# Kernel tuning notes

Measured on AMD Instinct MI355X. Metric: run time of the kernel, lower is better.

Reference implementation:

```python
import jax, jax.numpy as jnp
import numpy as np

INPUT_SIZE = 1024
HIDDEN_SIZE = 2048
BATCH = 4096


def _xavier(key, shape):
    fan_out, fan_in = shape
    std = jnp.sqrt(2.0 / (fan_in + fan_out)).astype(jnp.float32)
    return jax.random.normal(key, shape, dtype=jnp.float32) * std


def setup_inputs() -> dict:
    key = jax.random.key(0)
    ks = jax.random.split(key, 8)
    return {
        "x": jax.random.normal(ks[0], (BATCH, INPUT_SIZE), dtype=jnp.float32),
        "hprev": jax.random.normal(ks[1], (BATCH, HIDDEN_SIZE), dtype=jnp.float32),
        "Wh": _xavier(ks[2], (HIDDEN_SIZE, INPUT_SIZE)),
        "Wz": _xavier(ks[3], (HIDDEN_SIZE, INPUT_SIZE)),
        "Wr": _xavier(ks[4], (HIDDEN_SIZE, INPUT_SIZE)),
        "Uh": _xavier(ks[5], (HIDDEN_SIZE, HIDDEN_SIZE)),
        "Uz": _xavier(ks[6], (HIDDEN_SIZE, HIDDEN_SIZE)),
        "Ur": _xavier(ks[7], (HIDDEN_SIZE, HIDDEN_SIZE)),
        "bh": jnp.zeros((HIDDEN_SIZE,), dtype=jnp.float32),
        "bz": jnp.zeros((HIDDEN_SIZE,), dtype=jnp.float32),
        "br": jnp.zeros((HIDDEN_SIZE,), dtype=jnp.float32),
    }


def reference(x, hprev, Wh, Wz, Wr, Uh, Uz, Ur, bh, bz, br):
    # batched matvec: (b,i) @ (h,i)^T -> (b,h)
    r = jax.nn.sigmoid(x @ Wr.T + hprev @ Ur.T + br)
    z = jax.nn.sigmoid(x @ Wz.T + hprev @ Uz.T + bz)
    h_proposed = jnp.tanh(x @ Wh.T + (r * hprev) @ Uh.T + bh)
    return z * h_proposed + (1.0 - z) * hprev
```

## Files before the change

kernel.cpp:

```cpp
#include <hip/hip_runtime.h>

#define BATCH 4096
#define ISZ   1024
#define HSZ   2048

typedef __bf16 bf16x8 __attribute__((ext_vector_type(8)));
typedef float  f32x4  __attribute__((ext_vector_type(4)));

__device__ __forceinline__ unsigned short f2bf(float f) {
  unsigned u = __builtin_bit_cast(unsigned, f);
  u += 0x7fffu + ((u >> 16) & 1u);
  return (unsigned short)(u >> 16);
}
__device__ __forceinline__ float bf2f(unsigned short s) {
  unsigned u = ((unsigned)s) << 16;
  return __builtin_bit_cast(float, u);
}

struct CvtArgs {
  const float* src[6];
  unsigned short* dst[6];
  int cum[7];
};

__global__ __launch_bounds__(256) void cvt_all_kernel(CvtArgs a, int total4) {
  int i = blockIdx.x * 256 + threadIdx.x;
  if (i >= total4) return;
  int s = 0;
#pragma unroll
  for (int k = 0; k < 5; ++k) s += (i >= a.cum[k + 1]) ? 1 : 0;
  int off = i - a.cum[s];
  float4 f = ((const float4*)a.src[s])[off];
  ushort4 o;
  o.x = f2bf(f.x); o.y = f2bf(f.y); o.z = f2bf(f.z); o.w = f2bf(f.w);
  ((ushort4*)a.dst[s])[off] = o;
}

__device__ __forceinline__ void stage_tile64(const unsigned short* __restrict__ g, int ldK,
                                             int tileRow, int k0, char* lds, int t) {
  char* l0 = lds + ((t >> 6) << 10);
#pragma unroll
  for (int k = 0; k < 4; ++k) {
    int linear = t + k * 256;
    int row = linear >> 3;
    int cs  = linear & 7;
    int c   = cs ^ (row & 7);
    const unsigned short* gp = g + (size_t)(tileRow + row) * ldK + (k0 + c * 8);
    __builtin_amdgcn_global_load_lds((const __attribute__((address_space(1))) void*)gp,
                                     (__attribute__((address_space(3))) void*)(l0 + k * 4096),
                                     16, 0, 0);
  }
}

__device__ __forceinline__ void stage_tile64_w8(const unsigned short* __restrict__ g, int ldK,
                                                int tileRow, int k0, char* lds, int t) {
  char* l0 = lds + ((t >> 6) << 10);
#pragma unroll
  for (int k = 0; k < 2; ++k) {
    int linear = t + k * 512;
    int row = linear >> 3;
    int cs  = linear & 7;
    int c   = cs ^ (row & 7);
    const unsigned short* gp = g + (size_t)(tileRow + row) * ldK + (k0 + c * 8);
    __builtin_amdgcn_global_load_lds((const __attribute__((address_space(1))) void*)gp,
                                     (__attribute__((address_space(3))) void*)(l0 + k * 8192),
                                     16, 0, 0);
  }
}

__device__ __forceinline__ void gemm_seg(const unsigned short* __restrict__ A,
                                         const unsigned short* __restrict__ W,
                                         int K, int rowBase, int colBase,
                                         char* ldsA, char* ldsB,
                                         f32x4 (&acc)[4][4], int t) {
  const int lane = t & 63;
  const int wid  = t >> 6;
  const int wm   = wid >> 1, wn = wid & 1;
  const int lrow = lane & 15;
  const int quad = lane >> 4;
  const int r7   = lrow & 7;
  for (int k0 = 0; k0 < K; k0 += 64) {
    stage_tile64(A, K, rowBase, k0, ldsA, t);
    stage_tile64(W, K, colBase, k0, ldsB, t);
    __syncthreads();
#pragma unroll
    for (int kk = 0; kk < 2; ++kk) {
      const int swz = (((kk << 2) | quad) ^ r7) * 16;
      bf16x8 af[4], bfr[4];
#pragma unroll
      for (int i = 0; i < 4; ++i) {
        af[i]  = *(const bf16x8*)(ldsA + (wm * 64 + i * 16 + lrow) * 128 + swz);
        bfr[i] = *(const bf16x8*)(ldsB + (wn * 64 + i * 16 + lrow) * 128 + swz);
      }
#pragma unroll
      for (int i = 0; i < 4; ++i)
#pragma unroll
        for (int j = 0; j < 4; ++j)
          acc[i][j] = __builtin_amdgcn_mfma_f32_16x16x32_bf16(af[i], bfr[j], acc[i][j], 0, 0, 0);
    }
    __syncthreads();
  }
}

__device__ __forceinline__ void gemm_seg8(const unsigned short* __restrict__ A,
                                          const unsigned short* __restrict__ W,
                                          int K, int rowBase, int colBase,
                                          char* ldsA, char* ldsB,
                                          f32x4 (&acc)[4][2], int t) {
  const int lane = t & 63;
  const int wid  = t >> 6;
  const int wm   = wid >> 2;
  const int wn   = wid & 3;
  const int lrow = lane & 15;
  const int quad = lane >> 4;
  const int r7   = lrow & 7;
  for (int k0 = 0; k0 < K; k0 += 64) {
    stage_tile64_w8(A, K, rowBase, k0, ldsA, t);
    stage_tile64_w8(W, K, colBase, k0, ldsB, t);
    __syncthreads();
#pragma unroll
    for (int kk = 0; kk < 2; ++kk) {
      const int swz = (((kk << 2) | quad) ^ r7) * 16;
      bf16x8 af[4], bfr[2];
#pragma unroll
      for (int i = 0; i < 4; ++i)
        af[i]  = *(const bf16x8*)(ldsA + (wm * 64 + i * 16 + lrow) * 128 + swz);
#pragma unroll
      for (int j = 0; j < 2; ++j)
        bfr[j] = *(const bf16x8*)(ldsB + (wn * 32 + j * 16 + lrow) * 128 + swz);
#pragma unroll
      for (int i = 0; i < 4; ++i)
#pragma unroll
        for (int j = 0; j < 2; ++j)
          acc[i][j] = __builtin_amdgcn_mfma_f32_16x16x32_bf16(af[i], bfr[j], acc[i][j], 0, 0, 0);
    }
    __syncthreads();
  }
}

__device__ __forceinline__ float fast_sigmoid(float v) {
  return 1.0f / (1.0f + __expf(-v));
}
__device__ __forceinline__ float fast_tanh(float v) {
  float e = __expf(2.0f * v);
  return 1.0f - 2.0f / (e + 1.0f);
}

__global__ __launch_bounds__(256, 4) void gate_rz(
    const unsigned short* __restrict__ xb, const unsigned short* __restrict__ hb,
    const unsigned short* __restrict__ Wr, const unsigned short* __restrict__ Ur,
    const unsigned short* __restrict__ Wz, const unsigned short* __restrict__ Uz,
    const float* __restrict__ br, const float* __restrict__ bz,
    const float* __restrict__ Wh32, const float* __restrict__ Uh32,
    unsigned short* __restrict__ Whb, unsigned short* __restrict__ Uhb,
    unsigned short* __restrict__ rh, unsigned short* __restrict__ Zbuf) {
  __shared__ char lds[32768];
  const int t = threadIdx.x;

  if (blockIdx.z == 0) {
    const int NW = (HSZ * ISZ) / 4;
    const int NU = (HSZ * HSZ) / 4;
    int tid = (blockIdx.x + (blockIdx.y << 4)) * 256 + t;
    for (int i = tid; i < NW + NU; i += 512 * 256) {
      const float4* s4 = (i < NW) ? (const float4*)Wh32 + i
                                  : (const float4*)Uh32 + (i - NW);
      ushort4* d4 = (i < NW) ? (ushort4*)Whb + i
                             : (ushort4*)Uhb + (i - NW);
      float4 f = *s4;
      ushort4 o;
      o.x = f2bf(f.x); o.y = f2bf(f.y); o.z = f2bf(f.z); o.w = f2bf(f.w);
      *d4 = o;
    }
    return;
  }

  char* ldsA = lds;
  char* ldsB = lds + 16384;
  int lin = blockIdx.x + (blockIdx.y << 4) + ((blockIdx.z - 1) << 9);
  int xcd = lin & 7, s = lin >> 3;
  int bx = xcd * 2 + (s & 1);
  int by = (s >> 1) & 31;
  int bz_ = s >> 6;

  const int rowBase = by * 128;
  const int colBase = bx * 128;
  const bool isZ = (bz_ != 0);
  const unsigned short* W = isZ ? Wz : Wr;
  const unsigned short* U = isZ ? Uz : Ur;
  const float* biasP = isZ ? bz : br;

  f32x4 acc[4][4];
#pragma unroll
  for (int i = 0; i < 4; ++i)
#pragma unroll
    for (int j = 0; j < 4; ++j)
      acc[i][j] = (f32x4){0.f, 0.f, 0.f, 0.f};

  gemm_seg(xb, W, ISZ, rowBase, colBase, ldsA, ldsB, acc, t);
  gemm_seg(hb, U, HSZ, rowBase, colBase, ldsA, ldsB, acc, t);

  const int lane = t & 63, wid = t >> 6;
  const int wm = wid >> 1, wn = wid & 1, lrow = lane & 15, quad = lane >> 4;
#pragma unroll
  for (int i = 0; i < 4; ++i) {
#pragma unroll
    for (int j = 0; j < 4; ++j) {
      int col = colBase + wn * 64 + j * 16 + lrow;
      float bv = biasP[col];
#pragma unroll
      for (int r = 0; r < 4; ++r) {
        int row = rowBase + wm * 64 + i * 16 + quad * 4 + r;
        float sg = fast_sigmoid(acc[i][j][r] + bv);
        int idx = row * HSZ + col;
        if (isZ) {
          Zbuf[idx] = f2bf(sg);
        } else {
          rh[idx] = f2bf(sg * bf2f(hb[idx]));
        }
      }
    }
  }
}

__global__ __launch_bounds__(512, 4) void gate_h(
    const unsigned short* __restrict__ xb, const unsigned short* __restrict__ rhb,
    const unsigned short* __restrict__ Wh, const unsigned short* __restrict__ Uh,
    const float* __restrict__ bh, const unsigned short* __restrict__ Zbuf,
    const float* __restrict__ hprev, float* __restrict__ out) {
  __shared__ char lds[32768];
  char* ldsA = lds;
  char* ldsB = lds + 16384;
  const int t = threadIdx.x;

  int lin = blockIdx.x + (blockIdx.y << 4);
  int xcd = lin & 7, s = lin >> 3;
  int bx = xcd * 2 + (s & 1);
  int by = s >> 1;

  const int rowBase = by * 128;
  const int colBase = bx * 128;

  f32x4 acc[4][2];
#pragma unroll
  for (int i = 0; i < 4; ++i)
#pragma unroll
    for (int j = 0; j < 2; ++j)
      acc[i][j] = (f32x4){0.f, 0.f, 0.f, 0.f};

  gemm_seg8(xb, Wh, ISZ, rowBase, colBase, ldsA, ldsB, acc, t);
  gemm_seg8(rhb, Uh, HSZ, rowBase, colBase, ldsA, ldsB, acc, t);

  const int lane = t & 63, wid = t >> 6;
  const int wm = wid >> 2, wn = wid & 3, lrow = lane & 15, quad = lane >> 4;
#pragma unroll
  for (int i = 0; i < 4; ++i) {
#pragma unroll
    for (int j = 0; j < 2; ++j) {
      int col = colBase + wn * 32 + j * 16 + lrow;
      float bv = bh[col];
#pragma unroll
      for (int r = 0; r < 4; ++r) {
        int row = rowBase + wm * 64 + i * 16 + quad * 4 + r;
        float hp = fast_tanh(acc[i][j][r] + bv);
        int idx = row * HSZ + col;
        float z = bf2f(Zbuf[idx]);
        float h = hprev[idx];
        out[idx] = h + z * (hp - h);
      }
    }
  }
}

extern "C" void kernel_launch(void* const* d_in, const int* in_sizes, int n_in,
                              void* d_out, int out_size, void* d_ws, size_t ws_size,
                              hipStream_t stream) {
  (void)in_sizes; (void)n_in; (void)out_size; (void)ws_size;
  const float* x     = (const float*)d_in[0];
  const float* hprev = (const float*)d_in[1];
  const float* Wh    = (const float*)d_in[2];
  const float* Wz    = (const float*)d_in[3];
  const float* Wr    = (const float*)d_in[4];
  const float* Uh    = (const float*)d_in[5];
  const float* Uz    = (const float*)d_in[6];
  const float* Ur    = (const float*)d_in[7];
  const float* bh    = (const float*)d_in[8];
  const float* bz    = (const float*)d_in[9];
  const float* br    = (const float*)d_in[10];
  float* out = (float*)d_out;

  char* ws = (char*)d_ws;
  size_t off = 0;
  auto alloc = [&](size_t bytes) { char* p = ws + off; off += bytes; return p; };
  unsigned short* xb  = (unsigned short*)alloc((size_t)BATCH * ISZ * 2);
  unsigned short* hb  = (unsigned short*)alloc((size_t)BATCH * HSZ * 2);
  unsigned short* Wrb = (unsigned short*)alloc((size_t)HSZ * ISZ * 2);
  unsigned short* Wzb = (unsigned short*)alloc((size_t)HSZ * ISZ * 2);
  unsigned short* Whb = (unsigned short*)alloc((size_t)HSZ * ISZ * 2);
  unsigned short* Urb = (unsigned short*)alloc((size_t)HSZ * HSZ * 2);
  unsigned short* Uzb = (unsigned short*)alloc((size_t)HSZ * HSZ * 2);
  unsigned short* Uhb = (unsigned short*)alloc((size_t)HSZ * HSZ * 2);
  unsigned short* rhb = (unsigned short*)alloc((size_t)BATCH * HSZ * 2);
  unsigned short* Zb  = (unsigned short*)alloc((size_t)BATCH * HSZ * 2);

  CvtArgs ca;
  const float* srcs[6]      = {x, hprev, Wr, Wz, Ur, Uz};
  unsigned short* dsts[6]   = {xb, hb, Wrb, Wzb, Urb, Uzb};
  int n4s[6] = {BATCH * ISZ / 4, BATCH * HSZ / 4,
                HSZ * ISZ / 4, HSZ * ISZ / 4,
                HSZ * HSZ / 4, HSZ * HSZ / 4};
  int cum = 0;
  for (int i = 0; i < 6; ++i) {
    ca.src[i] = srcs[i];
    ca.dst[i] = dsts[i];
    ca.cum[i] = cum;
    cum += n4s[i];
  }
  ca.cum[6] = cum;
  cvt_all_kernel<<<(cum + 255) / 256, 256, 0, stream>>>(ca, cum);

  dim3 gridA(HSZ / 128, BATCH / 128, 3);
  gate_rz<<<gridA, 256, 0, stream>>>(xb, hb, Wrb, Urb, Wzb, Uzb, br, bz,
                                     Wh, Uh, Whb, Uhb, rhb, Zb);

  dim3 gridB(HSZ / 128, BATCH / 128, 1);
  gate_h<<<gridB, 512, 0, stream>>>(xb, rhb, Whb, Uhb, bh, Zb, hprev, out);
}
```

Measured before the change: 340.3 us.

## Split gate_h GEMM along K into two partial kernels plus blend epilogue

The h-gate GEMM becomes a split-K kernel. Each output tile is computed by two 256-thread blocks: one covers the x·Wh part plus the first 512 of the Uh reduction, the other covers the remaining 1536. The fp32 partial sums go to two workspace buffers, and a separate elementwise blend kernel adds them with the bias, applies tanh and does the z-blend. This doubles the block count of the second GEMM (512 to 1024 blocks) to fill the GPU better, at the cost of writing and reading 64 MB of fp32 partials and an extra launch.

New measurement: 350.0 us. 2.8% more time.

```diff
diff --git a/kernel.cpp b/kernel.cpp
--- a/kernel.cpp
+++ b/kernel.cpp
@@ -52,25 +52,10 @@
   }
 }
 
-__device__ __forceinline__ void stage_tile64_w8(const unsigned short* __restrict__ g, int ldK,
-                                                int tileRow, int k0, char* lds, int t) {
-  char* l0 = lds + ((t >> 6) << 10);
-#pragma unroll
-  for (int k = 0; k < 2; ++k) {
-    int linear = t + k * 512;
-    int row = linear >> 3;
-    int cs  = linear & 7;
-    int c   = cs ^ (row & 7);
-    const unsigned short* gp = g + (size_t)(tileRow + row) * ldK + (k0 + c * 8);
-    __builtin_amdgcn_global_load_lds((const __attribute__((address_space(1))) void*)gp,
-                                     (__attribute__((address_space(3))) void*)(l0 + k * 8192),
-                                     16, 0, 0);
-  }
-}
-
 __device__ __forceinline__ void gemm_seg(const unsigned short* __restrict__ A,
                                          const unsigned short* __restrict__ W,
-                                         int K, int rowBase, int colBase,
+                                         int ldK, int kBeg, int kEnd,
+                                         int rowBase, int colBase,
                                          char* ldsA, char* ldsB,
                                          f32x4 (&acc)[4][4], int t) {
   const int lane = t & 63;
@@ -79,9 +64,9 @@
   const int lrow = lane & 15;
   const int quad = lane >> 4;
   const int r7   = lrow & 7;
-  for (int k0 = 0; k0 < K; k0 += 64) {
-    stage_tile64(A, K, rowBase, k0, ldsA, t);
-    stage_tile64(W, K, colBase, k0, ldsB, t);
+  for (int k0 = kBeg; k0 < kEnd; k0 += 64) {
+    stage_tile64(A, ldK, rowBase, k0, ldsA, t);
+    stage_tile64(W, ldK, colBase, k0, ldsB, t);
     __syncthreads();
 #pragma unroll
     for (int kk = 0; kk < 2; ++kk) {
@@ -96,42 +81,6 @@
       for (int i = 0; i < 4; ++i)
 #pragma unroll
         for (int j = 0; j < 4; ++j)
-          acc[i][j] = __builtin_amdgcn_mfma_f32_16x16x32_bf16(af[i], bfr[j], acc[i][j], 0, 0, 0);
-    }
-    __syncthreads();
-  }
-}
-
-__device__ __forceinline__ void gemm_seg8(const unsigned short* __restrict__ A,
-                                          const unsigned short* __restrict__ W,
-                                          int K, int rowBase, int colBase,
-                                          char* ldsA, char* ldsB,
-                                          f32x4 (&acc)[4][2], int t) {
-  const int lane = t & 63;
-  const int wid  = t >> 6;
-  const int wm   = wid >> 2;
-  const int wn   = wid & 3;
-  const int lrow = lane & 15;
-  const int quad = lane >> 4;
-  const int r7   = lrow & 7;
-  for (int k0 = 0; k0 < K; k0 += 64) {
-    stage_tile64_w8(A, K, rowBase, k0, ldsA, t);
-    stage_tile64_w8(W, K, colBase, k0, ldsB, t);
-    __syncthreads();
-#pragma unroll
-    for (int kk = 0; kk < 2; ++kk) {
-      const int swz = (((kk << 2) | quad) ^ r7) * 16;
-      bf16x8 af[4], bfr[2];
-#pragma unroll
-      for (int i = 0; i < 4; ++i)
-        af[i]  = *(const bf16x8*)(ldsA + (wm * 64 + i * 16 + lrow) * 128 + swz);
-#pragma unroll
-      for (int j = 0; j < 2; ++j)
-        bfr[j] = *(const bf16x8*)(ldsB + (wn * 32 + j * 16 + lrow) * 128 + swz);
-#pragma unroll
-      for (int i = 0; i < 4; ++i)
-#pragma unroll
-        for (int j = 0; j < 2; ++j)
           acc[i][j] = __builtin_amdgcn_mfma_f32_16x16x32_bf16(af[i], bfr[j], acc[i][j], 0, 0, 0);
     }
     __syncthreads();
@@ -196,8 +145,8 @@
     for (int j = 0; j < 4; ++j)
       acc[i][j] = (f32x4){0.f, 0.f, 0.f, 0.f};
 
-  gemm_seg(xb, W, ISZ, rowBase, colBase, ldsA, ldsB, acc, t);
-  gemm_seg(hb, U, HSZ, rowBase, colBase, ldsA, ldsB, acc, t);
+  gemm_seg(xb, W, ISZ, 0, ISZ, rowBase, colBase, ldsA, ldsB, acc, t);
+  gemm_seg(hb, U, HSZ, 0, HSZ, rowBase, colBase, ldsA, ldsB, acc, t);
 
   const int lane = t & 63, wid = t >> 6;
   const int wm = wid >> 1, wn = wid & 1, lrow = lane & 15, quad = lane >> 4;
@@ -222,11 +171,10 @@
   }
 }
 
-__global__ __launch_bounds__(512, 4) void gate_h(
+__global__ __launch_bounds__(256, 4) void gate_hk(
     const unsigned short* __restrict__ xb, const unsigned short* __restrict__ rhb,
     const unsigned short* __restrict__ Wh, const unsigned short* __restrict__ Uh,
-    const float* __restrict__ bh, const unsigned short* __restrict__ Zbuf,
-    const float* __restrict__ hprev, float* __restrict__ out) {
+    float* __restrict__ P0, float* __restrict__ P1) {
   __shared__ char lds[32768];
   char* ldsA = lds;
   char* ldsB = lds + 16384;
@@ -239,36 +187,68 @@
 
   const int rowBase = by * 128;
   const int colBase = bx * 128;
-
-  f32x4 acc[4][2];
+  const int kz = blockIdx.z;
+
+  f32x4 acc[4][4];
 #pragma unroll
   for (int i = 0; i < 4; ++i)
 #pragma unroll
-    for (int j = 0; j < 2; ++j)
+    for (int j = 0; j < 4; ++j)
       acc[i][j] = (f32x4){0.f, 0.f, 0.f, 0.f};
 
-  gemm_seg8(xb, Wh, ISZ, rowBase, colBase, ldsA, ldsB, acc, t);
-  gemm_seg8(rhb, Uh, HSZ, rowBase, colBase, ldsA, ldsB, acc, t);
-
+  if (kz == 0) {
+    gemm_seg(xb,  Wh, ISZ, 0, ISZ,    rowBase, colBase, ldsA, ldsB, acc, t);
+    gemm_seg(rhb, Uh, HSZ, 0, 512,    rowBase, colBase, ldsA, ldsB, acc, t);
+  } else {
+    gemm_seg(rhb, Uh, HSZ, 512, HSZ,  rowBase, colBase, ldsA, ldsB, acc, t);
+  }
+
+  float* P = (kz == 0) ? P0 : P1;
   const int lane = t & 63, wid = t >> 6;
-  const int wm = wid >> 2, wn = wid & 3, lrow = lane & 15, quad = lane >> 4;
+  const int wm = wid >> 1, wn = wid & 1, lrow = lane & 15, quad = lane >> 4;
 #pragma unroll
   for (int i = 0; i < 4; ++i) {
 #pragma unroll
-    for (int j = 0; j < 2; ++j) {
-      int col = colBase + wn * 32 + j * 16 + lrow;
-      float bv = bh[col];
+    for (int j = 0; j < 4; ++j) {
+      int col = colBase + wn * 64 + j * 16 + lrow;
 #pragma unroll
       for (int r = 0; r < 4; ++r) {
         int row = rowBase + wm * 64 + i * 16 + quad * 4 + r;
-        float hp = fast_tanh(acc[i][j][r] + bv);
-        int idx = row * HSZ + col;
-        float z = bf2f(Zbuf[idx]);
-        float h = hprev[idx];
-        out[idx] = h + z * (hp - h);
+        P[row * HSZ + col] = acc[i][j][r];
       }
     }
   }
+}
+
+__global__ __launch_bounds__(256) void blend_kernel(
+    const float* __restrict__ P0, const float* __restrict__ P1,
+    const float* __restrict__ bh, const unsigned short* __restrict__ Zbuf,
+    const float* __restrict__ hprev, float* __restrict__ out, int n4) {
+  int i = blockIdx.x * 256 + threadIdx.x;
+  if (i >= n4) return;
+  float4 p0 = ((const float4*)P0)[i];
+  float4 p1 = ((const float4*)P1)[i];
+  float4 bv = *(const float4*)(bh + ((i * 4) & (HSZ - 1)));
+  ushort4 zb = ((const ushort4*)Zbuf)[i];
+  float4 h  = ((const float4*)hprev)[i];
+  float4 o;
+  {
+    float hp = fast_tanh(p0.x + p1.x + bv.x); float z = bf2f(zb.x);
+    o.x = h.x + z * (hp - h.x);
+  }
+  {
+    float hp = fast_tanh(p0.y + p1.y + bv.y); float z = bf2f(zb.y);
+    o.y = h.y + z * (hp - h.y);
+  }
+  {
+    float hp = fast_tanh(p0.z + p1.z + bv.z); float z = bf2f(zb.z);
+    o.z = h.z + z * (hp - h.z);
+  }
+  {
+    float hp = fast_tanh(p0.w + p1.w + bv.w); float z = bf2f(zb.w);
+    o.w = h.w + z * (hp - h.w);
+  }
+  ((float4*)out)[i] = o;
 }
 
 extern "C" void kernel_launch(void* const* d_in, const int* in_sizes, int n_in,
@@ -301,6 +281,8 @@
   unsigned short* Uhb = (unsigned short*)alloc((size_t)HSZ * HSZ * 2);
   unsigned short* rhb = (unsigned short*)alloc((size_t)BATCH * HSZ * 2);
   unsigned short* Zb  = (unsigned short*)alloc((size_t)BATCH * HSZ * 2);
+  float*          P0  = (float*)alloc((size_t)BATCH * HSZ * 4);
+  float*          P1  = (float*)alloc((size_t)BATCH * HSZ * 4);
 
   CvtArgs ca;
   const float* srcs[6]      = {x, hprev, Wr, Wz, Ur, Uz};
@@ -322,6 +304,9 @@
   gate_rz<<<gridA, 256, 0, stream>>>(xb, hb, Wrb, Urb, Wzb, Uzb, br, bz,
                                      Wh, Uh, Whb, Uhb, rhb, Zb);
 
-  dim3 gridB(HSZ / 128, BATCH / 128, 1);
-  gate_h<<<gridB, 512, 0, stream>>>(xb, rhb, Whb, Uhb, bh, Zb, hprev, out);
-}
+  dim3 gridB(HSZ / 128, BATCH / 128, 2);
+  gate_hk<<<gridB, 256, 0, stream>>>(xb, rhb, Whb, Uhb, P0, P1);
+
+  int n4 = BATCH * HSZ / 4;
+  blend_kernel<<<(n4 + 255) / 256, 256, 0, stream>>>(P0, P1, bh, Zb, hprev, out, n4);
+}
```
